# Performance work log

Measured on AMD Instinct MI355X. Metric: run time of the kernel, lower is better.

## Reference

```python
import jax, jax.numpy as jnp
import numpy as np

L_MAX = 3
N_RADIAL = [2, 2, 1, 1]  # radial powers r^{2k} with 2k+l <= l_max=3


def fibonacci_sphere(n):
    i = np.arange(n, dtype=np.float64)
    phi = np.pi * (3.0 - np.sqrt(5.0))
    y = 1.0 - 2.0 * i / (n - 1)
    r = np.sqrt(np.maximum(1.0 - y * y, 0.0))
    th = phi * i
    pts = np.stack([np.cos(th) * r, y, np.sin(th) * r], -1)
    return jnp.asarray(pts, dtype=jnp.float32)


def real_sh(u):
    # real spherical harmonics on unit vectors u[...,3], degrees 0..3
    x, y, z = u[..., 0], u[..., 1], u[..., 2]
    Y0 = 0.28209479 * jnp.ones_like(x)[..., None]
    Y1 = 0.48860251 * jnp.stack([y, z, x], -1)
    Y2 = jnp.stack([
        1.09254843 * x * y,
        1.09254843 * y * z,
        0.31539157 * (3.0 * z * z - 1.0),
        1.09254843 * x * z,
        0.54627421 * (x * x - y * y)], -1)
    Y3 = jnp.stack([
        0.59004359 * y * (3.0 * x * x - y * y),
        2.89061144 * x * y * z,
        0.45704579 * y * (5.0 * z * z - 1.0),
        0.37317633 * z * (5.0 * z * z - 3.0),
        0.45704579 * x * (5.0 * z * z - 1.0),
        1.44530572 * z * (x * x - y * y),
        0.59004359 * x * (x * x - 3.0 * y * y)], -1)
    return [Y0, Y1, Y2, Y3]


def grid_sample_3d(vol, grid):
    # vol: [B, D, H, W]; grid: [B, d, h, w, 3], grid[...,0]->W, [...,1]->H, [...,2]->D
    # align_corners=True, zeros padding (torch.nn.functional.grid_sample semantics)
    B, Dv, Hv, Wv = vol.shape
    ix = (grid[..., 0] + 1.0) * 0.5 * (Wv - 1)
    iy = (grid[..., 1] + 1.0) * 0.5 * (Hv - 1)
    iz = (grid[..., 2] + 1.0) * 0.5 * (Dv - 1)
    x0f, y0f, z0f = jnp.floor(ix), jnp.floor(iy), jnp.floor(iz)
    wx, wy, wz = ix - x0f, iy - y0f, iz - z0f
    x0, y0, z0 = x0f.astype(jnp.int32), y0f.astype(jnp.int32), z0f.astype(jnp.int32)
    x1, y1, z1 = x0 + 1, y0 + 1, z0 + 1
    bidx = jnp.arange(B).reshape(B, 1, 1, 1)

    def tap(zi, yi, xi):
        m = ((zi >= 0) & (zi < Dv) & (yi >= 0) & (yi < Hv) & (xi >= 0) & (xi < Wv)).astype(vol.dtype)
        v = vol[bidx, jnp.clip(zi, 0, Dv - 1), jnp.clip(yi, 0, Hv - 1), jnp.clip(xi, 0, Wv - 1)]
        return v * m

    out = (tap(z0, y0, x0) * (1 - wz) * (1 - wy) * (1 - wx)
         + tap(z0, y0, x1) * (1 - wz) * (1 - wy) * wx
         + tap(z0, y1, x0) * (1 - wz) * wy * (1 - wx)
         + tap(z0, y1, x1) * (1 - wz) * wy * wx
         + tap(z1, y0, x0) * wz * (1 - wy) * (1 - wx)
         + tap(z1, y0, x1) * wz * (1 - wy) * wx
         + tap(z1, y1, x0) * wz * wy * (1 - wx)
         + tap(z1, y1, x1) * wz * wy * wx)
    return out


def setup_inputs() -> dict:
    key = jax.random.key(0)
    ks = jax.random.split(key, 12)
    B, H, W, D, S = 8, 32, 32, 32, 64
    x = jax.random.normal(ks[0], (B, H, W, D, 3), jnp.float32) * 0.35
    x_density = jax.random.uniform(ks[1], (B, H, W, D), jnp.float32)
    F = jax.random.normal(ks[2], (B, S, 256), jnp.float32) * 0.1
    def lin(k, i, o):
        return jax.random.normal(k, (i, o), jnp.float32) / np.sqrt(i)
    return {
        'x': x, 'x_density': x_density, 'F': F,
        'S2': fibonacci_sphere(S),
        'bw1': lin(ks[3], 256, 64), 'bb1': jnp.zeros((64,), jnp.float32),
        'bw2': lin(ks[4], 64, 3), 'bb2': jnp.zeros((3,), jnp.float32),
        'cw1': lin(ks[5], 256, 128), 'cb1': jnp.zeros((128,), jnp.float32),
        'cw2': lin(ks[6], 128, 64), 'cb2': jnp.zeros((64,), jnp.float32),
        'iw': lin(ks[7], 128, 3), 'ib': jnp.zeros((3,), jnp.float32),
    }


def reference(x, x_density, F, S2, bw1, bb1, bw2, bb2, cw1, cb1, cw2, cb2, iw, ib):
    B, H, W, D, _ = x.shape
    S = S2.shape[0]
    quad = (4.0 * jnp.pi) / S  # sphere quadrature weight for fibonacci samples
    Ybase = real_sh(S2)  # list of [S, 2l+1]

    # frame (E) branch: basis MLP -> type-1 SH coefficients -> normalize
    basis = jax.nn.relu(F @ bw1 + bb1) @ bw2 + bb2          # [B,S,3]
    E = jnp.einsum('vm,bvc->bmc', Ybase[1], basis) * quad   # [B,3,3]
    E = E / jnp.clip(jnp.linalg.norm(E, axis=-1, keepdims=True), 1e-6)

    # latent code branch: code MLP -> full SHT coefficients per degree l
    latent = jax.nn.relu(F @ cw1 + cb1) @ cw2 + cb2         # [B,S,64]
    coeffs = [jnp.einsum('vm,bvc->bmc', Ybase[l], latent) * quad for l in range(L_MAX + 1)]

    # zernike monomials of the grid points
    xf = x.reshape(B, -1, 3)                                # [B,V,3]
    r = jnp.linalg.norm(xf, axis=-1, keepdims=True)         # [B,V,1]
    u = xf / jnp.clip(r, 1e-6)
    Yx = real_sh(u)
    points_code = []
    points_inv = None
    for l in range(L_MAX + 1):
        Pl = Yx[l] * (r ** l)                               # solid harmonic [B,V,2l+1]
        rad = jnp.stack([r[..., 0] ** (2 * k) for k in range(N_RADIAL[l])], -1)  # [B,V,n_l]
        zl = Pl[..., :, None] * rad[..., None, :]           # [B,V,2l+1,n_l]
        p = jnp.einsum('bmi,bvmj->bvij', coeffs[l], zl)     # [B,V,64,n_l]
        p = p.reshape(B, p.shape[1], -1)
        points_code.append(p)
        if l == 1:
            points_inv = p                                  # [B,V,128]
    points_code = jnp.concatenate(points_code, -1)          # [B,V,384]

    pts = points_inv @ iw + ib                              # [B,V,3]
    coords = pts.reshape(B, H, W, D, 3)
    vol = x_density.reshape(B, H, W, D)
    sampled = grid_sample_3d(vol, coords)                   # [B,H,W,D]
    return sampled, E, coords, points_code
```

## Files before the change

kernel.cpp:

```cpp
#include <hip/hip_runtime.h>
#include <math.h>

#define OFF_E     262144
#define OFF_COORD 262216
#define OFF_CODE  1048648

#define QUAD 0.19634954084936207f

#define WS_H1 0
#define WS_H2 32768
#define WS_C  98304
#define WS_AB 106496

__global__ __launch_bounds__(384) void k_hidden(
    const float* __restrict__ F,
    const float* __restrict__ bw1, const float* __restrict__ bb1,
    const float* __restrict__ cw1, const float* __restrict__ cb1,
    float* __restrict__ ws)
{
    __shared__ float sF[8 * 257];
    const int blk = blockIdx.x;
    const int b   = blk >> 3;
    const int r0  = (blk & 7) * 8;
    const int tid = threadIdx.x;

    float* wsH1 = ws + WS_H1;
    float* wsH2 = ws + WS_H2;

    const float* Fb = F + ((size_t)b * 64 + r0) * 256;
    for (int i = tid; i < 2048; i += 384) sF[(i >> 8) * 257 + (i & 255)] = Fb[i];
    __syncthreads();

    if (tid < 128) {
        const int row = tid >> 4, k4 = (tid & 15) * 4;
        const float* fr = sF + row * 257;
        float4 acc = *(const float4*)&bb1[k4];
        #pragma unroll 4
        for (int j = 0; j < 256; ++j) {
            const float  f = fr[j];
            const float4 w = *(const float4*)&bw1[j * 64 + k4];
            acc.x = fmaf(f, w.x, acc.x);
            acc.y = fmaf(f, w.y, acc.y);
            acc.z = fmaf(f, w.z, acc.z);
            acc.w = fmaf(f, w.w, acc.w);
        }
        acc.x = fmaxf(acc.x, 0.f); acc.y = fmaxf(acc.y, 0.f);
        acc.z = fmaxf(acc.z, 0.f); acc.w = fmaxf(acc.w, 0.f);
        *(float4*)&wsH1[((size_t)b * 64 + r0 + row) * 64 + k4] = acc;
    } else {
        const int tt  = tid - 128;
        const int row = tt >> 5, k4 = (tt & 31) * 4;
        const float* fr = sF + row * 257;
        float4 acc = *(const float4*)&cb1[k4];
        #pragma unroll 4
        for (int j = 0; j < 256; ++j) {
            const float  f = fr[j];
            const float4 w = *(const float4*)&cw1[j * 128 + k4];
            acc.x = fmaf(f, w.x, acc.x);
            acc.y = fmaf(f, w.y, acc.y);
            acc.z = fmaf(f, w.z, acc.z);
            acc.w = fmaf(f, w.w, acc.w);
        }
        acc.x = fmaxf(acc.x, 0.f); acc.y = fmaxf(acc.y, 0.f);
        acc.z = fmaxf(acc.z, 0.f); acc.w = fmaxf(acc.w, 0.f);
        *(float4*)&wsH2[((size_t)b * 64 + r0 + row) * 128 + k4] = acc;
    }
}

__global__ __launch_bounds__(512) void k_coeffs(
    const float* __restrict__ ws_in,
    const float* __restrict__ S2,
    const float* __restrict__ bw2, const float* __restrict__ bb2,
    const float* __restrict__ cw2, const float* __restrict__ cb2,
    const float* __restrict__ iw,
    float* __restrict__ ws_out, float* __restrict__ outE)
{
    __shared__ float sH2[64 * 129];
    __shared__ alignas(16) float sLat[64 * 64];
    __shared__ float sY[64 * 16];
    __shared__ float sBas[64 * 3];
    __shared__ float sC[16 * 64];
    __shared__ float sE[9];

    const int b = blockIdx.x, tid = threadIdx.x;
    const float* wsH1 = ws_in + WS_H1;
    const float* wsH2 = ws_in + WS_H2;
    float* wsC  = ws_out + WS_C;
    float* wsAB = ws_out + WS_AB;

    const float* H2b = wsH2 + (size_t)b * 8192;
    for (int i = tid; i < 8192; i += 512) sH2[(i >> 7) * 129 + (i & 127)] = H2b[i];

    if (tid < 64) {
        const float x = S2[tid * 3 + 0], y = S2[tid * 3 + 1], z = S2[tid * 3 + 2];
        float* Yv = sY + tid * 16;
        Yv[0]  = 0.28209479f;
        Yv[1]  = 0.48860251f * y;
        Yv[2]  = 0.48860251f * z;
        Yv[3]  = 0.48860251f * x;
        Yv[4]  = 1.09254843f * x * y;
        Yv[5]  = 1.09254843f * y * z;
        Yv[6]  = 0.31539157f * (3.f * z * z - 1.f);
        Yv[7]  = 1.09254843f * x * z;
        Yv[8]  = 0.54627421f * (x * x - y * y);
        Yv[9]  = 0.59004359f * y * (3.f * x * x - y * y);
        Yv[10] = 2.89061144f * x * y * z;
        Yv[11] = 0.45704579f * y * (5.f * z * z - 1.f);
        Yv[12] = 0.37317633f * z * (5.f * z * z - 3.f);
        Yv[13] = 0.45704579f * x * (5.f * z * z - 1.f);
        Yv[14] = 1.44530572f * z * (x * x - y * y);
        Yv[15] = 0.59004359f * x * (x * x - 3.f * y * y);
    }

    float breg = 0.f;
    if (tid < 192) {
        const int v = tid / 3, c = tid % 3;
        const float* h1 = wsH1 + ((size_t)b * 64 + v) * 64;
        float acc = bb2[c];
        #pragma unroll 8
        for (int k = 0; k < 64; ++k) acc = fmaf(h1[k], bw2[k * 3 + c], acc);
        breg = acc;
    }
    __syncthreads();

    if (tid < 192) sBas[tid] = breg;

    for (int t = tid; t < 1024; t += 512) {
        const int row = t >> 4, i4 = (t & 15) * 4;
        const float* h2 = sH2 + row * 129;
        float4 acc = *(const float4*)&cb2[i4];
        #pragma unroll 4
        for (int k = 0; k < 128; ++k) {
            const float  h = h2[k];
            const float4 w = *(const float4*)&cw2[k * 64 + i4];
            acc.x = fmaf(h, w.x, acc.x);
            acc.y = fmaf(h, w.y, acc.y);
            acc.z = fmaf(h, w.z, acc.z);
            acc.w = fmaf(h, w.w, acc.w);
        }
        *(float4*)&sLat[row * 64 + i4] = acc;
    }
    __syncthreads();

    for (int o = tid; o < 1024; o += 512) {
        const int m = o >> 6, i = o & 63;
        float acc = 0.f;
        #pragma unroll 8
        for (int v = 0; v < 64; ++v) acc = fmaf(sY[v * 16 + m], sLat[v * 64 + i], acc);
        acc *= QUAD;
        sC[o] = acc;
        wsC[(size_t)b * 1024 + o] = acc;
    }
    if (tid < 9) {
        const int m = tid / 3, c = tid % 3;
        float acc = 0.f;
        for (int v = 0; v < 64; ++v) acc = fmaf(sY[v * 16 + 1 + m], sBas[v * 3 + c], acc);
        sE[tid] = acc * QUAD;
    }
    __syncthreads();

    if (tid < 9) {
        const int m = tid / 3;
        const float e0 = sE[m * 3 + 0], e1 = sE[m * 3 + 1], e2 = sE[m * 3 + 2];
        const float n = sqrtf(e0 * e0 + e1 * e1 + e2 * e2);
        outE[b * 9 + tid] = sE[tid] / fmaxf(n, 1e-6f);
    }
    if (tid < 18) {
        const int which = tid / 9, mc = tid % 9;
        const int m = mc / 3, c = mc % 3;
        float acc = 0.f;
        #pragma unroll 8
        for (int i = 0; i < 64; ++i)
            acc = fmaf(sC[(1 + m) * 64 + i], iw[(2 * i + which) * 3 + c], acc);
        wsAB[b * 18 + tid] = acc;
    }
}

__global__ __launch_bounds__(384) void k_points(
    const float* __restrict__ x, const float* __restrict__ dens,
    const float* __restrict__ ws, const float* __restrict__ ib,
    float* __restrict__ out)
{
    __shared__ alignas(16) float sC[16 * 64];
    __shared__ float sAB[18];
    __shared__ alignas(16) float sZ[128 * 20];

    const int blk = blockIdx.x;
    const int b   = blk >> 8;
    const int v0  = (blk & 255) * 128;
    const int tid = threadIdx.x;

    const float* wsC  = ws + WS_C;
    const float* wsAB = ws + WS_AB;

    if (tid < 256) ((float4*)sC)[tid] = ((const float4*)(wsC + (size_t)b * 1024))[tid];
    if (tid < 18) sAB[tid] = wsAB[b * 18 + tid];

    float z1 = 0.f, z2 = 0.f, z3 = 0.f, r2 = 0.f;
    size_t g = 0;
    if (tid < 128) {
        const int v = v0 + tid;
        g = (size_t)b * 32768 + v;
        const float px = x[g * 3 + 0], py = x[g * 3 + 1], pz = x[g * 3 + 2];
        r2 = px * px + py * py + pz * pz;
        const float r   = sqrtf(r2);
        const float inv = 1.f / fmaxf(r, 1e-6f);
        const float ux = px * inv, uy = py * inv, uz = pz * inv;
        float* Z = sZ + tid * 20;
        z1 = 0.48860251f * uy * r;
        z2 = 0.48860251f * uz * r;
        z3 = 0.48860251f * ux * r;
        Z[0] = z1; Z[1] = z2; Z[2] = z3; Z[3] = r2;
        const float r3 = r2 * r;
        Z[4]  = 0.59004359f * uy * (3.f * ux * ux - uy * uy) * r3;
        Z[5]  = 2.89061144f * ux * uy * uz * r3;
        Z[6]  = 0.45704579f * uy * (5.f * uz * uz - 1.f) * r3;
        Z[7]  = 0.37317633f * uz * (5.f * uz * uz - 3.f) * r3;
        Z[8]  = 0.45704579f * ux * (5.f * uz * uz - 1.f) * r3;
        Z[9]  = 1.44530572f * uz * (ux * ux - uy * uy) * r3;
        Z[10] = 0.59004359f * ux * (ux * ux - 3.f * uy * uy) * r3;
        Z[12] = 1.09254843f * ux * uy * r2;
        Z[13] = 1.09254843f * uy * uz * r2;
        Z[14] = 0.31539157f * (3.f * uz * uz - 1.f) * r2;
        Z[15] = 1.09254843f * ux * uz * r2;
        Z[16] = 0.54627421f * (ux * ux - uy * uy) * r2;
    }
    __syncthreads();

    const size_t rowbase = OFF_CODE + ((size_t)b * 32768 + v0) * 384;
    if (tid < 64) {
        const int q = tid & 31, h = tid >> 5;
        const float ca = sC[2 * q]     * 0.28209479f;
        const float cb = sC[2 * q + 1] * 0.28209479f;
        const float* zr = sZ + h * 20 + 3;
        float* po = out + rowbase + (size_t)h * 384 + 4 * q;
        #pragma unroll 8
        for (int vi = 0; vi < 64; ++vi) {
            const float r2v = zr[vi * 40];
            float4 o; o.x = ca; o.y = ca * r2v; o.z = cb; o.w = cb * r2v;
            *(float4*)po = o;
            po += 768;
        }
    } else if (tid < 128) {
        const int u = tid - 64, q = u & 31, h = u >> 5;
        const float c00 = sC[64 + 2 * q],     c01 = sC[128 + 2 * q],     c02 = sC[192 + 2 * q];
        const float c10 = sC[64 + 2 * q + 1], c11 = sC[128 + 2 * q + 1], c12 = sC[192 + 2 * q + 1];
        const float* zr = sZ + h * 20;
        float* po = out + rowbase + (size_t)h * 384 + 128 + 4 * q;
        #pragma unroll 8
        for (int vi = 0; vi < 64; ++vi) {
            const float4 z = *(const float4*)(zr + vi * 40);
            float d0 = c00 * z.x; d0 = fmaf(c01, z.y, d0); d0 = fmaf(c02, z.z, d0);
            float d1 = c10 * z.x; d1 = fmaf(c11, z.y, d1); d1 = fmaf(c12, z.z, d1);
            float4 o; o.x = d0; o.y = d0 * z.w; o.z = d1; o.w = d1 * z.w;
            *(float4*)po = o;
            po += 768;
        }
    } else if (tid < 256) {
        const int q = tid & 15, s = (tid - 128) >> 4;
        const int i0 = 4 * q;
        const float4 cf0 = *(const float4*)&sC[4 * 64 + i0];
        const float4 cf1 = *(const float4*)&sC[5 * 64 + i0];
        const float4 cf2 = *(const float4*)&sC[6 * 64 + i0];
        const float4 cf3 = *(const float4*)&sC[7 * 64 + i0];
        const float4 cf4 = *(const float4*)&sC[8 * 64 + i0];
        const float* zr = sZ + s * 20;
        float* po = out + rowbase + (size_t)s * 384 + 256 + i0;
        #pragma unroll 4
        for (int vi = 0; vi < 16; ++vi) {
            const float4 za = *(const float4*)(zr + vi * 160 + 12);
            const float  zb = zr[vi * 160 + 16];
            float a0 = cf0.x * za.x, a1 = cf0.y * za.x, a2 = cf0.z * za.x, a3 = cf0.w * za.x;
            a0 = fmaf(cf1.x, za.y, a0); a1 = fmaf(cf1.y, za.y, a1);
            a2 = fmaf(cf1.z, za.y, a2); a3 = fmaf(cf1.w, za.y, a3);
            a0 = fmaf(cf2.x, za.z, a0); a1 = fmaf(cf2.y, za.z, a1);
            a2 = fmaf(cf2.z, za.z, a2); a3 = fmaf(cf2.w, za.z, a3);
            a0 = fmaf(cf3.x, za.w, a0); a1 = fmaf(cf3.y, za.w, a1);
            a2 = fmaf(cf3.z, za.w, a2); a3 = fmaf(cf3.w, za.w, a3);
            a0 = fmaf(cf4.x, zb, a0);   a1 = fmaf(cf4.y, zb, a1);
            a2 = fmaf(cf4.z, zb, a2);   a3 = fmaf(cf4.w, zb, a3);
            float4 o; o.x = a0; o.y = a1; o.z = a2; o.w = a3;
            *(float4*)po = o;
            po += 3072;
        }
    } else {
        const int q = tid & 15, s = (tid - 256) >> 4;
        const int i0 = 4 * q;
        const float4 cf0 = *(const float4*)&sC[ 9 * 64 + i0];
        const float4 cf1 = *(const float4*)&sC[10 * 64 + i0];
        const float4 cf2 = *(const float4*)&sC[11 * 64 + i0];
        const float4 cf3 = *(const float4*)&sC[12 * 64 + i0];
        const float4 cf4 = *(const float4*)&sC[13 * 64 + i0];
        const float4 cf5 = *(const float4*)&sC[14 * 64 + i0];
        const float4 cf6 = *(const float4*)&sC[15 * 64 + i0];
        const float* zr = sZ + s * 20;
        float* po = out + rowbase + (size_t)s * 384 + 320 + i0;
        #pragma unroll 4
        for (int vi = 0; vi < 16; ++vi) {
            const float4 za = *(const float4*)(zr + vi * 160 + 4);
            const float2 zb = *(const float2*)(zr + vi * 160 + 8);
            const float  zc = zr[vi * 160 + 10];
            float a0 = cf0.x * za.x, a1 = cf0.y * za.x, a2 = cf0.z * za.x, a3 = cf0.w * za.x;
            a0 = fmaf(cf1.x, za.y, a0); a1 = fmaf(cf1.y, za.y, a1);
            a2 = fmaf(cf1.z, za.y, a2); a3 = fmaf(cf1.w, za.y, a3);
            a0 = fmaf(cf2.x, za.z, a0); a1 = fmaf(cf2.y, za.z, a1);
            a2 = fmaf(cf2.z, za.z, a2); a3 = fmaf(cf2.w, za.z, a3);
            a0 = fmaf(cf3.x, za.w, a0); a1 = fmaf(cf3.y, za.w, a1);
            a2 = fmaf(cf3.z, za.w, a2); a3 = fmaf(cf3.w, za.w, a3);
            a0 = fmaf(cf4.x, zb.x, a0); a1 = fmaf(cf4.y, zb.x, a1);
            a2 = fmaf(cf4.z, zb.x, a2); a3 = fmaf(cf4.w, zb.x, a3);
            a0 = fmaf(cf5.x, zb.y, a0); a1 = fmaf(cf5.y, zb.y, a1);
            a2 = fmaf(cf5.z, zb.y, a2); a3 = fmaf(cf5.w, zb.y, a3);
            a0 = fmaf(cf6.x, zc, a0);   a1 = fmaf(cf6.y, zc, a1);
            a2 = fmaf(cf6.z, zc, a2);   a3 = fmaf(cf6.w, zc, a3);
            float4 o; o.x = a0; o.y = a1; o.z = a2; o.w = a3;
            *(float4*)po = o;
            po += 3072;
        }
    }

    if (tid < 128) {
        const float zr0 = z1, zr1 = z2, zr2 = z3;
        float pt[3];
        #pragma unroll
        for (int cc = 0; cc < 3; ++cc) {
            float acc = ib[cc];
            acc = fmaf(zr0, sAB[0 * 3 + cc] + r2 * sAB[9 + 0 * 3 + cc], acc);
            acc = fmaf(zr1, sAB[1 * 3 + cc] + r2 * sAB[9 + 1 * 3 + cc], acc);
            acc = fmaf(zr2, sAB[2 * 3 + cc] + r2 * sAB[9 + 2 * 3 + cc], acc);
            pt[cc] = acc;
            out[OFF_COORD + g * 3 + cc] = acc;
        }

        const float ix = (pt[0] + 1.f) * 0.5f * 31.f;
        const float iy = (pt[1] + 1.f) * 0.5f * 31.f;
        const float iz = (pt[2] + 1.f) * 0.5f * 31.f;
        const float x0f = floorf(ix), y0f = floorf(iy), z0f = floorf(iz);
        const float wx = ix - x0f, wy = iy - y0f, wz = iz - z0f;
        const int x0 = (int)x0f, y0 = (int)y0f, z0 = (int)z0f;
        const float* volb = dens + (size_t)b * 32768;
        float s = 0.f;
        #pragma unroll
        for (int dz = 0; dz < 2; ++dz) {
            const int zi = z0 + dz;
            const float wzz = dz ? wz : 1.f - wz;
            #pragma unroll
            for (int dy = 0; dy < 2; ++dy) {
                const int yi = y0 + dy;
                const float wyy = dy ? wy : 1.f - wy;
                #pragma unroll
                for (int dx = 0; dx < 2; ++dx) {
                    const int xi = x0 + dx;
                    const float wxx = dx ? wx : 1.f - wx;
                    if (zi >= 0 && zi < 32 && yi >= 0 && yi < 32 && xi >= 0 && xi < 32)
                        s += wzz * wyy * wxx * volb[zi * 1024 + yi * 32 + xi];
                }
            }
        }
        out[g] = s;
    }
}

extern "C" void kernel_launch(void* const* d_in, const int* in_sizes, int n_in,
                              void* d_out, int out_size, void* d_ws, size_t ws_size,
                              hipStream_t stream) {
    const float* x    = (const float*)d_in[0];
    const float* dens = (const float*)d_in[1];
    const float* F    = (const float*)d_in[2];
    const float* S2   = (const float*)d_in[3];
    const float* bw1  = (const float*)d_in[4];
    const float* bb1  = (const float*)d_in[5];
    const float* bw2  = (const float*)d_in[6];
    const float* bb2  = (const float*)d_in[7];
    const float* cw1  = (const float*)d_in[8];
    const float* cb1  = (const float*)d_in[9];
    const float* cw2  = (const float*)d_in[10];
    const float* cb2  = (const float*)d_in[11];
    const float* iw   = (const float*)d_in[12];
    const float* ib   = (const float*)d_in[13];
    float* out = (float*)d_out;
    float* ws  = (float*)d_ws;

    k_hidden<<<64,   384, 0, stream>>>(F, bw1, bb1, cw1, cb1, ws);
    k_coeffs<<<8,    512, 0, stream>>>(ws, S2, bw2, bb2, cw2, cb2, iw, ws, out + OFF_E);
    k_points<<<2048, 384, 0, stream>>>(x, dens, ws, ib, out);
}
```

Measured before the change: 551.0 us.

## Split point kernel into monomial-plane precompute and coalesced code expansion

```diff
diff --git a/kernel.cpp b/kernel.cpp
--- a/kernel.cpp
+++ b/kernel.cpp
@@ -11,6 +11,8 @@
 #define WS_H2 32768
 #define WS_C  98304
 #define WS_AB 106496
+#define WS_ZT 110592
+#define ZT_PER_B (16 * 32768)
 
 __global__ __launch_bounds__(384) void k_hidden(
     const float* __restrict__ F,
@@ -173,6 +175,192 @@
         for (int i = 0; i < 64; ++i)
             acc = fmaf(sC[(1 + m) * 64 + i], iw[(2 * i + which) * 3 + c], acc);
         wsAB[b * 18 + tid] = acc;
+    }
+}
+
+__global__ __launch_bounds__(256) void k_zplanes(
+    const float* __restrict__ x, const float* __restrict__ dens,
+    const float* __restrict__ ib, float* __restrict__ ws,
+    float* __restrict__ out)
+{
+    const int g = blockIdx.x * 256 + threadIdx.x;
+    const int b = g >> 15, v = g & 32767;
+
+    const float px = x[(size_t)g * 3 + 0];
+    const float py = x[(size_t)g * 3 + 1];
+    const float pz = x[(size_t)g * 3 + 2];
+    const float r2 = px * px + py * py + pz * pz;
+    const float r   = sqrtf(r2);
+    const float inv = 1.f / fmaxf(r, 1e-6f);
+    const float ux = px * inv, uy = py * inv, uz = pz * inv;
+
+    float* zt = ws + WS_ZT + (size_t)b * ZT_PER_B + v;
+    const float z1 = 0.48860251f * uy * r;
+    const float z2 = 0.48860251f * uz * r;
+    const float z3 = 0.48860251f * ux * r;
+    zt[0 * 32768] = z1;
+    zt[1 * 32768] = z2;
+    zt[2 * 32768] = z3;
+    zt[3 * 32768] = r2;
+    const float r3 = r2 * r;
+    zt[4 * 32768]  = 0.59004359f * uy * (3.f * ux * ux - uy * uy) * r3;
+    zt[5 * 32768]  = 2.89061144f * ux * uy * uz * r3;
+    zt[6 * 32768]  = 0.45704579f * uy * (5.f * uz * uz - 1.f) * r3;
+    zt[7 * 32768]  = 0.37317633f * uz * (5.f * uz * uz - 3.f) * r3;
+    zt[8 * 32768]  = 0.45704579f * ux * (5.f * uz * uz - 1.f) * r3;
+    zt[9 * 32768]  = 1.44530572f * uz * (ux * ux - uy * uy) * r3;
+    zt[10 * 32768] = 0.59004359f * ux * (ux * ux - 3.f * uy * uy) * r3;
+    zt[11 * 32768] = 1.09254843f * ux * uy * r2;
+    zt[12 * 32768] = 1.09254843f * uy * uz * r2;
+    zt[13 * 32768] = 0.31539157f * (3.f * uz * uz - 1.f) * r2;
+    zt[14 * 32768] = 1.09254843f * ux * uz * r2;
+    zt[15 * 32768] = 0.54627421f * (ux * ux - uy * uy) * r2;
+
+    const float* AB = ws + WS_AB + b * 18;
+    float pt[3];
+    #pragma unroll
+    for (int cc = 0; cc < 3; ++cc) {
+        float acc = ib[cc];
+        acc = fmaf(z1, AB[0 + cc] + r2 * AB[9 + cc], acc);
+        acc = fmaf(z2, AB[3 + cc] + r2 * AB[12 + cc], acc);
+        acc = fmaf(z3, AB[6 + cc] + r2 * AB[15 + cc], acc);
+        pt[cc] = acc;
+        out[OFF_COORD + (size_t)g * 3 + cc] = acc;
+    }
+
+    const float ixf = (pt[0] + 1.f) * 0.5f * 31.f;
+    const float iyf = (pt[1] + 1.f) * 0.5f * 31.f;
+    const float izf = (pt[2] + 1.f) * 0.5f * 31.f;
+    const float x0f = floorf(ixf), y0f = floorf(iyf), z0f = floorf(izf);
+    const float wx = ixf - x0f, wy = iyf - y0f, wz = izf - z0f;
+    const int x0 = (int)x0f, y0 = (int)y0f, z0 = (int)z0f;
+    const float* volb = dens + (size_t)b * 32768;
+    float s = 0.f;
+    #pragma unroll
+    for (int dz = 0; dz < 2; ++dz) {
+        const int zi = z0 + dz;
+        const float wzz = dz ? wz : 1.f - wz;
+        #pragma unroll
+        for (int dy = 0; dy < 2; ++dy) {
+            const int yi = y0 + dy;
+            const float wyy = dy ? wy : 1.f - wy;
+            #pragma unroll
+            for (int dx = 0; dx < 2; ++dx) {
+                const int xi = x0 + dx;
+                const float wxx = dx ? wx : 1.f - wx;
+                if (zi >= 0 && zi < 32 && yi >= 0 && yi < 32 && xi >= 0 && xi < 32)
+                    s += wzz * wyy * wxx * volb[zi * 1024 + yi * 32 + xi];
+            }
+        }
+    }
+    out[g] = s;
+}
+
+__global__ __launch_bounds__(384) void k_expand(
+    const float* __restrict__ ws, float* __restrict__ out)
+{
+    const int blk   = blockIdx.x;
+    const int b     = blk & 7;
+    const int vbase = (blk >> 3) * 64;
+    const int tid   = threadIdx.x;
+    const int q     = tid % 96;
+    const int dv    = tid / 96;
+
+    const float* C  = ws + WS_C + b * 1024;
+    const float* zt = ws + WS_ZT + (size_t)b * ZT_PER_B + vbase + dv;
+    float* po = out + OFF_CODE + ((size_t)(b * 32768 + vbase + dv)) * 384 + 4 * q;
+
+    if (q < 32) {
+        const float ca = C[2 * q]     * 0.28209479f;
+        const float cb = C[2 * q + 1] * 0.28209479f;
+        const float* zr2 = zt + 3 * 32768;
+        #pragma unroll 8
+        for (int p = 0; p < 16; ++p) {
+            const float r2 = zr2[p * 4];
+            float4 o; o.x = ca; o.y = ca * r2; o.z = cb; o.w = cb * r2;
+            *(float4*)(po + (size_t)p * 1536) = o;
+        }
+    } else if (q < 64) {
+        const int u = q - 32;
+        const float c00 = C[64 + 2 * u],     c01 = C[128 + 2 * u],     c02 = C[192 + 2 * u];
+        const float c10 = C[64 + 2 * u + 1], c11 = C[128 + 2 * u + 1], c12 = C[192 + 2 * u + 1];
+        const float* za = zt;
+        const float* zb = zt + 32768;
+        const float* zc = zt + 65536;
+        const float* zr2 = zt + 98304;
+        #pragma unroll 8
+        for (int p = 0; p < 16; ++p) {
+            const float a = za[p * 4], bb = zb[p * 4], cc = zc[p * 4], r2 = zr2[p * 4];
+            float d0 = c00 * a; d0 = fmaf(c01, bb, d0); d0 = fmaf(c02, cc, d0);
+            float d1 = c10 * a; d1 = fmaf(c11, bb, d1); d1 = fmaf(c12, cc, d1);
+            float4 o; o.x = d0; o.y = d0 * r2; o.z = d1; o.w = d1 * r2;
+            *(float4*)(po + (size_t)p * 1536) = o;
+        }
+    } else if (q < 80) {
+        const int i0 = 4 * (q - 64);
+        const float4 cf0 = *(const float4*)&C[4 * 64 + i0];
+        const float4 cf1 = *(const float4*)&C[5 * 64 + i0];
+        const float4 cf2 = *(const float4*)&C[6 * 64 + i0];
+        const float4 cf3 = *(const float4*)&C[7 * 64 + i0];
+        const float4 cf4 = *(const float4*)&C[8 * 64 + i0];
+        const float* p0 = zt + 11 * 32768;
+        const float* p1 = zt + 12 * 32768;
+        const float* p2 = zt + 13 * 32768;
+        const float* p3 = zt + 14 * 32768;
+        const float* p4 = zt + 15 * 32768;
+        #pragma unroll 4
+        for (int p = 0; p < 16; ++p) {
+            const float t0 = p0[p * 4], t1 = p1[p * 4], t2 = p2[p * 4];
+            const float t3 = p3[p * 4], t4 = p4[p * 4];
+            float a0 = cf0.x * t0, a1 = cf0.y * t0, a2 = cf0.z * t0, a3 = cf0.w * t0;
+            a0 = fmaf(cf1.x, t1, a0); a1 = fmaf(cf1.y, t1, a1);
+            a2 = fmaf(cf1.z, t1, a2); a3 = fmaf(cf1.w, t1, a3);
+            a0 = fmaf(cf2.x, t2, a0); a1 = fmaf(cf2.y, t2, a1);
+            a2 = fmaf(cf2.z, t2, a2); a3 = fmaf(cf2.w, t2, a3);
+            a0 = fmaf(cf3.x, t3, a0); a1 = fmaf(cf3.y, t3, a1);
+            a2 = fmaf(cf3.z, t3, a2); a3 = fmaf(cf3.w, t3, a3);
+            a0 = fmaf(cf4.x, t4, a0); a1 = fmaf(cf4.y, t4, a1);
+            a2 = fmaf(cf4.z, t4, a2); a3 = fmaf(cf4.w, t4, a3);
+            float4 o; o.x = a0; o.y = a1; o.z = a2; o.w = a3;
+            *(float4*)(po + (size_t)p * 1536) = o;
+        }
+    } else {
+        const int i0 = 4 * (q - 80);
+        const float4 cf0 = *(const float4*)&C[ 9 * 64 + i0];
+        const float4 cf1 = *(const float4*)&C[10 * 64 + i0];
+        const float4 cf2 = *(const float4*)&C[11 * 64 + i0];
+        const float4 cf3 = *(const float4*)&C[12 * 64 + i0];
+        const float4 cf4 = *(const float4*)&C[13 * 64 + i0];
+        const float4 cf5 = *(const float4*)&C[14 * 64 + i0];
+        const float4 cf6 = *(const float4*)&C[15 * 64 + i0];
+        const float* p0 = zt + 4 * 32768;
+        const float* p1 = zt + 5 * 32768;
+        const float* p2 = zt + 6 * 32768;
+        const float* p3 = zt + 7 * 32768;
+        const float* p4 = zt + 8 * 32768;
+        const float* p5 = zt + 9 * 32768;
+        const float* p6 = zt + 10 * 32768;
+        #pragma unroll 4
+        for (int p = 0; p < 16; ++p) {
+            const float t0 = p0[p * 4], t1 = p1[p * 4], t2 = p2[p * 4];
+            const float t3 = p3[p * 4], t4 = p4[p * 4], t5 = p5[p * 4];
+            const float t6 = p6[p * 4];
+            float a0 = cf0.x * t0, a1 = cf0.y * t0, a2 = cf0.z * t0, a3 = cf0.w * t0;
+            a0 = fmaf(cf1.x, t1, a0); a1 = fmaf(cf1.y, t1, a1);
+            a2 = fmaf(cf1.z, t1, a2); a3 = fmaf(cf1.w, t1, a3);
+            a0 = fmaf(cf2.x, t2, a0); a1 = fmaf(cf2.y, t2, a1);
+            a2 = fmaf(cf2.z, t2, a2); a3 = fmaf(cf2.w, t2, a3);
+            a0 = fmaf(cf3.x, t3, a0); a1 = fmaf(cf3.y, t3, a1);
+            a2 = fmaf(cf3.z, t3, a2); a3 = fmaf(cf3.w, t3, a3);
+            a0 = fmaf(cf4.x, t4, a0); a1 = fmaf(cf4.y, t4, a1);
+            a2 = fmaf(cf4.z, t4, a2); a3 = fmaf(cf4.w, t4, a3);
+            a0 = fmaf(cf5.x, t5, a0); a1 = fmaf(cf5.y, t5, a1);
+            a2 = fmaf(cf5.z, t5, a2); a3 = fmaf(cf5.w, t5, a3);
+            a0 = fmaf(cf6.x, t6, a0); a1 = fmaf(cf6.y, t6, a1);
+            a2 = fmaf(cf6.z, t6, a2); a3 = fmaf(cf6.w, t6, a3);
+            float4 o; o.x = a0; o.y = a1; o.z = a2; o.w = a3;
+            *(float4*)(po + (size_t)p * 1536) = o;
+        }
     }
 }
 
@@ -381,7 +569,14 @@
     float* out = (float*)d_out;
     float* ws  = (float*)d_ws;
 
-    k_hidden<<<64,   384, 0, stream>>>(F, bw1, bb1, cw1, cb1, ws);
-    k_coeffs<<<8,    512, 0, stream>>>(ws, S2, bw2, bb2, cw2, cb2, iw, ws, out + OFF_E);
-    k_points<<<2048, 384, 0, stream>>>(x, dens, ws, ib, out);
+    k_hidden<<<64, 384, 0, stream>>>(F, bw1, bb1, cw1, cb1, ws);
+    k_coeffs<<<8,  512, 0, stream>>>(ws, S2, bw2, bb2, cw2, cb2, iw, ws, out + OFF_E);
+
+    const size_t ws_needed = (size_t)(WS_ZT + 8 * ZT_PER_B) * sizeof(float);
+    if (ws_size >= ws_needed) {
+        k_zplanes<<<1024, 256, 0, stream>>>(x, dens, ib, ws, out);
+        k_expand<<<4096,  384, 0, stream>>>(ws, out);
+    } else {
+        k_points<<<2048,  384, 0, stream>>>(x, dens, ws, ib, out);
+    }
 }
```

New measurement: 557.8 us. Within noise of the previous version (+1.2%).
